# Performance work log

Measured on AMD Instinct MI355X. Metric: run time of the kernel, lower is better.

## Reference

```python
import jax, jax.numpy as jnp
import numpy as np

N_NODES = 50000
N_EDGES = 800000
IN_CH = 256
HID = 64
HEADS = 4
OUT_CH = 4
NEG_SLOPE = 0.2


def _add_self_loops(edge_index, n):
    ar = jnp.arange(n, dtype=edge_index.dtype)
    loops = jnp.stack([ar, ar])
    return jnp.concatenate([edge_index, loops], axis=1)


def _gat_conv(x, edge_index, W, att_src, att_dst, bias, heads, ch):
    # PyG GATConv (no edge features, add_self_loops=True, concat=True)
    n = x.shape[0]
    ei = _add_self_loops(edge_index, n)
    src, dst = ei[0], ei[1]
    xp = (x @ W).reshape(n, heads, ch)            # [N,H,C]
    a_src = (xp * att_src).sum(-1)                 # [N,H]
    a_dst = (xp * att_dst).sum(-1)                 # [N,H]
    alpha = jax.nn.leaky_relu(a_src[src] + a_dst[dst], NEG_SLOPE)  # [E',H]
    amax = jax.ops.segment_max(alpha, dst, num_segments=n)
    alpha = jnp.exp(alpha - amax[dst])
    denom = jax.ops.segment_sum(alpha, dst, num_segments=n)
    alpha = alpha / (denom[dst] + 1e-16)
    msg = xp[src] * alpha[:, :, None]              # [E',H,C]
    out = jax.ops.segment_sum(msg, dst, num_segments=n)  # [N,H,C]
    return out.reshape(n, heads * ch) + bias


def setup_inputs() -> dict:
    key = jax.random.key(0)
    ks = jax.random.split(key, 12)
    x = jax.random.normal(ks[0], (N_NODES, IN_CH), dtype=jnp.float32)
    edge_index = jax.random.randint(ks[1], (2, N_EDGES), 0, N_NODES, dtype=jnp.int64)
    w = jax.random.uniform(ks[2], (N_EDGES,), dtype=jnp.float32)
    s1 = 1.0 / np.sqrt(IN_CH)
    s2 = 1.0 / np.sqrt(HEADS * HID)
    return {
        "x": x, "edge_index": edge_index, "w": w,
        "W1": jax.random.normal(ks[3], (IN_CH, HEADS * HID), dtype=jnp.float32) * s1,
        "att_src1": jax.random.normal(ks[4], (1, HEADS, HID), dtype=jnp.float32) * s2,
        "att_dst1": jax.random.normal(ks[5], (1, HEADS, HID), dtype=jnp.float32) * s2,
        "b1": jnp.zeros((HEADS * HID,), dtype=jnp.float32),
        "W2": jax.random.normal(ks[6], (HEADS * HID, HID), dtype=jnp.float32) * s2,
        "att_src2": jax.random.normal(ks[7], (1, 1, HID), dtype=jnp.float32) * s2,
        "att_dst2": jax.random.normal(ks[8], (1, 1, HID), dtype=jnp.float32) * s2,
        "b2": jnp.zeros((HID,), dtype=jnp.float32),
        "Wc": jax.random.normal(ks[9], (2 * HID, OUT_CH), dtype=jnp.float32) * (1.0 / np.sqrt(2 * HID)),
        "bc": jnp.zeros((OUT_CH,), dtype=jnp.float32),
    }


def reference(x, edge_index, w, W1, att_src1, att_dst1, b1,
              W2, att_src2, att_dst2, b2, Wc, bc):
    # w (edge_attr) is ignored: GATConv was built without edge_dim, so no lin_edge.
    h = _gat_conv(x, edge_index, W1, att_src1, att_dst1, b1, HEADS, HID)
    h = jax.nn.relu(h)
    h = _gat_conv(h, edge_index, W2, att_src2, att_dst2, b2, 1, HID)
    row, col = edge_index[0], edge_index[1]
    edge_emb = jnp.concatenate([h[row], h[col]], axis=-1)  # [E, 2*HID]
    return edge_emb @ Wc + bc
```

## Files before the change

### kernel.cpp

```cpp
#include <hip/hip_runtime.h>


#define NEG 0.2f

typedef __attribute__((ext_vector_type(8))) short bf16x8;
typedef __attribute__((ext_vector_type(4))) float f32x4;

__device__ __forceinline__ unsigned short f2bf(float f) {
    unsigned int u = __float_as_uint(f);
    unsigned int r = (u + 0x7FFFu + ((u >> 16) & 1u)) >> 16;
    return (unsigned short)r;
}
__device__ __forceinline__ float bf2f(unsigned short h) {
    return __uint_as_float(((unsigned int)h) << 16);
}
__device__ __forceinline__ float bflo(unsigned int u) { return __uint_as_float(u << 16); }
__device__ __forceinline__ float bfhi(unsigned int u) { return __uint_as_float(u & 0xFFFF0000u); }
__device__ __forceinline__ float lrelu(float x) { return x > 0.f ? x : NEG * x; }

__device__ __forceinline__ void async16(const void* g, void* l) {
    __builtin_amdgcn_global_load_lds(
        (const __attribute__((address_space(1))) unsigned int*)g,
        (__attribute__((address_space(3))) unsigned int*)l, 16, 0, 0);
}


__global__ __launch_bounds__(256) void k_init(int* deg, int* cur, int n) {
    int i = blockIdx.x * 256 + threadIdx.x;
    if (i < n) { deg[i] = 1; cur[i] = 0; }
}

__global__ __launch_bounds__(256) void k_hist(const int* __restrict__ ei, int* deg, int E) {
    int e = blockIdx.x * 256 + threadIdx.x;
    if (e < E) atomicAdd(&deg[ei[E + e]], 1);
}

__global__ __launch_bounds__(256) void k_bsum(const int* __restrict__ deg, int* __restrict__ bsum, int n) {
    int i = blockIdx.x * 256 + threadIdx.x;
    int v = (i < n) ? deg[i] : 0;
#pragma unroll
    for (int off = 1; off < 64; off <<= 1) v += __shfl_xor(v, off, 64);
    __shared__ int ws[4];
    int wv = threadIdx.x >> 6, l = threadIdx.x & 63;
    if (l == 0) ws[wv] = v;
    __syncthreads();
    if (threadIdx.x == 0) bsum[blockIdx.x] = ws[0] + ws[1] + ws[2] + ws[3];
}

__global__ __launch_bounds__(256) void k_bscan(const int* __restrict__ bsum, int* __restrict__ boff,
                                               int* __restrict__ rowptr, int nb, int n) {
    __shared__ int s[256];
    int t = threadIdx.x;
    int v = (t < nb) ? bsum[t] : 0;
    s[t] = v;
    __syncthreads();
    for (int off = 1; off < 256; off <<= 1) {
        int u = (t >= off) ? s[t - off] : 0;
        __syncthreads();
        s[t] += u;
        __syncthreads();
    }
    if (t < nb) boff[t] = s[t] - v;
    if (t == nb - 1) rowptr[n] = s[t];
}

__global__ __launch_bounds__(256) void k_rowptr(const int* __restrict__ deg, const int* __restrict__ boff,
                                                int* __restrict__ rowptr, int n) {
    __shared__ int s[256];
    int i = blockIdx.x * 256 + threadIdx.x;
    int t = threadIdx.x;
    int v = (i < n) ? deg[i] : 0;
    s[t] = v;
    __syncthreads();
    for (int off = 1; off < 256; off <<= 1) {
        int u = (t >= off) ? s[t - off] : 0;
        __syncthreads();
        s[t] += u;
        __syncthreads();
    }
    if (i < n) rowptr[i] = boff[blockIdx.x] + s[t] - v;
}

__global__ __launch_bounds__(256) void k_scatter(const int* __restrict__ ei, const int* __restrict__ rowptr,
                                                 int* cur, int* csr_src, int E, int N) {
    int e = blockIdx.x * 256 + threadIdx.x;
    if (e < E) {
        int d = ei[E + e];
        int pos = rowptr[d] + atomicAdd(&cur[d], 1);
        csr_src[pos] = ei[e];
    } else if (e < E + N) {
        int i = e - E;
        int pos = rowptr[i] + atomicAdd(&cur[i], 1);
        csr_src[pos] = i;
    }
}


__global__ __launch_bounds__(256) void k_pack_hi(const float* __restrict__ src,
                                                 unsigned short* __restrict__ hi, long n4) {
    long i = (long)blockIdx.x * 256 + threadIdx.x;
    long stride = (long)gridDim.x * 256;
    for (; i < n4; i += stride) {
        float4 v = ((const float4*)src)[i];
        ((ushort4*)hi)[i] = make_ushort4(f2bf(v.x), f2bf(v.y), f2bf(v.z), f2bf(v.w));
    }
}

__global__ __launch_bounds__(256) void k_pack_w2(const float* __restrict__ W1,
                                                 const float* __restrict__ W2,
                                                 unsigned short* __restrict__ W1hT,
                                                 unsigned short* __restrict__ W1lT,
                                                 unsigned short* __restrict__ W2hT,
                                                 unsigned short* __restrict__ W2lT) {
    int t = blockIdx.x * 256 + threadIdx.x;
    if (t < 256 * 256) {
        int n = t >> 8, k = t & 255;
        float v = W1[k * 256 + n];
        unsigned short h = f2bf(v);
        W1hT[t] = h;
        W1lT[t] = f2bf(v - bf2f(h));
    } else {
        int t2 = t - 256 * 256;
        if (t2 < 64 * 256) {
            int n = t2 >> 8, k = t2 & 255;
            float v = W2[k * 64 + n];
            unsigned short h = f2bf(v);
            W2hT[t2] = h;
            W2lT[t2] = f2bf(v - bf2f(h));
        }
    }
}

template<int WGM, int WGN>
__global__ __launch_bounds__(256, 2) void k_gemm_lds(const unsigned short* __restrict__ Ah,
                                                     const unsigned short* __restrict__ BhT,
                                                     const unsigned short* __restrict__ BlT,
                                                     unsigned short* __restrict__ Cb, int M, int N, int K,
                                                     const float* __restrict__ att_s,
                                                     const float* __restrict__ att_d,
                                                     float* __restrict__ as, float* __restrict__ ad, int H) {
    constexpr int BM = WGM * 64, BN = WGN * 64;
    __shared__ char lds[BM * 128 + BN * 256];
    char* LAh = lds;
    char* LBh = lds + BM * 128;
    char* LBl = lds + BM * 128 + BN * 128;

    const int t = threadIdx.x, wv = t >> 6, l = t & 63;
    const int r = l & 15, hk = l >> 4;
    const int m0 = blockIdx.x * BM;
    const int n0 = blockIdx.y * BN;
    const int wr = wv / WGN, wc = wv % WGN;
    const int wrow0 = wr * 64, wcol0 = wc * 64;

    f32x4 acc[4][4];
#pragma unroll
    for (int i = 0; i < 4; i++)
#pragma unroll
        for (int j = 0; j < 4; j++) acc[i][j] = f32x4{0, 0, 0, 0};

    const int lrow8 = l >> 3;
    const int cbs = ((l & 7) ^ lrow8) << 4;
    const size_t K2 = (size_t)K * 2;
    const int NCH = K >> 6;

    for (int c = 0; c < NCH; ++c) {
        const int kk2 = c * 128;
        {
            const int SA = BM / 8;
            for (int i = wv; i < SA; i += 4) {
                int row = i * 8 + lrow8;
                size_t go = (size_t)(m0 + row) * K2 + kk2 + cbs;
                async16((const char*)Ah + go, LAh + i * 1024);
            }
            const int SB = BN / 8;
            for (int i = wv; i < SB; i += 4) {
                int row = i * 8 + lrow8;
                size_t go = (size_t)(n0 + row) * K2 + kk2 + cbs;
                async16((const char*)BhT + go, LBh + i * 1024);
                async16((const char*)BlT + go, LBl + i * 1024);
            }
        }
        __syncthreads();
#pragma unroll
        for (int ks = 0; ks < 2; ++ks) {
            const int cb = ks * 64 + hk * 16;
            bf16x8 a_h[4], b_h[4], b_l[4];
#pragma unroll
            for (int fm = 0; fm < 4; ++fm) {
                int row = wrow0 + fm * 16 + r;
                int ad_ = row * 128 + (cb ^ ((row & 7) << 4));
                a_h[fm] = *(const bf16x8*)(LAh + ad_);
            }
#pragma unroll
            for (int fn = 0; fn < 4; ++fn) {
                int row = wcol0 + fn * 16 + r;
                int ad_ = row * 128 + (cb ^ ((row & 7) << 4));
                b_h[fn] = *(const bf16x8*)(LBh + ad_);
                b_l[fn] = *(const bf16x8*)(LBl + ad_);
            }
#pragma unroll
            for (int fm = 0; fm < 4; ++fm)
#pragma unroll
                for (int fn = 0; fn < 4; ++fn) {
                    acc[fm][fn] = __builtin_amdgcn_mfma_f32_16x16x32_bf16(a_h[fm], b_h[fn], acc[fm][fn], 0, 0, 0);
                    acc[fm][fn] = __builtin_amdgcn_mfma_f32_16x16x32_bf16(a_h[fm], b_l[fn], acc[fm][fn], 0, 0, 0);
                }
        }
        if (c + 1 < NCH) __syncthreads();
    }

#pragma unroll
    for (int fm = 0; fm < 4; ++fm)
#pragma unroll
        for (int fn = 0; fn < 4; ++fn)
#pragma unroll
            for (int j = 0; j < 4; ++j) {
                int m = m0 + wrow0 + fm * 16 + hk * 4 + j;
                if (m < M) Cb[(size_t)m * N + n0 + wcol0 + fn * 16 + r] = f2bf(acc[fm][fn][j]);
            }

    {
        int head = (n0 + wcol0) >> 6;
        float satt[4], datt[4];
#pragma unroll
        for (int fn = 0; fn < 4; ++fn) {
            satt[fn] = att_s[head * 64 + fn * 16 + r];
            datt[fn] = att_d[head * 64 + fn * 16 + r];
        }
#pragma unroll
        for (int fm = 0; fm < 4; ++fm)
#pragma unroll
            for (int j = 0; j < 4; ++j) {
                float ps = 0.f, pd = 0.f;
#pragma unroll
                for (int fn = 0; fn < 4; ++fn) {
                    ps += satt[fn] * acc[fm][fn][j];
                    pd += datt[fn] * acc[fm][fn][j];
                }
#pragma unroll
                for (int off = 1; off <= 8; off <<= 1) {
                    ps += __shfl_xor(ps, off, 64);
                    pd += __shfl_xor(pd, off, 64);
                }
                if (r == 0) {
                    int m = m0 + wrow0 + fm * 16 + hk * 4 + j;
                    if (m < M) { as[m * H + head] = ps; ad[m * H + head] = pd; }
                }
            }
    }
}


__global__ __launch_bounds__(256) void k_gather1(const unsigned short* __restrict__ xpb,
                                                 const float* __restrict__ as, const float* __restrict__ ad,
                                                 const int* __restrict__ rowptr, const int* __restrict__ csr_src,
                                                 const float* __restrict__ b1,
                                                 unsigned short* __restrict__ h1h, int M) {
    int wv = threadIdx.x >> 6, lane = threadIdx.x & 63;
    int n = blockIdx.x * 4 + wv;
    if (n >= M) return;
    int half = lane >> 5;
    int q = lane & 31;
    int h = q >> 3;
    float adv = ad[n * 4 + h];
    int start = rowptr[n], end = rowptr[n + 1];
    float acc[8] = {0.f, 0.f, 0.f, 0.f, 0.f, 0.f, 0.f, 0.f};
    float den = 0.f;

    auto edge = [&](int s, uint4 v) {
        float p = __expf(lrelu(as[s * 4 + h] + adv));
        den += p;
        acc[0] += p * bflo(v.x); acc[1] += p * bfhi(v.x);
        acc[2] += p * bflo(v.y); acc[3] += p * bfhi(v.y);
        acc[4] += p * bflo(v.z); acc[5] += p * bfhi(v.z);
        acc[6] += p * bflo(v.w); acc[7] += p * bfhi(v.w);
    };

    int e = start;
    for (; e + 7 < end; e += 8) {
        int sa = csr_src[e + half];
        int sb = csr_src[e + 2 + half];
        int sc = csr_src[e + 4 + half];
        int sd = csr_src[e + 6 + half];
        uint4 va = *(const uint4*)(xpb + (size_t)sa * 256 + q * 8);
        uint4 vb = *(const uint4*)(xpb + (size_t)sb * 256 + q * 8);
        uint4 vc = *(const uint4*)(xpb + (size_t)sc * 256 + q * 8);
        uint4 vd = *(const uint4*)(xpb + (size_t)sd * 256 + q * 8);
        edge(sa, va); edge(sb, vb); edge(sc, vc); edge(sd, vd);
    }
    if (e + 3 < end) {
        int sa = csr_src[e + half];
        int sb = csr_src[e + 2 + half];
        uint4 va = *(const uint4*)(xpb + (size_t)sa * 256 + q * 8);
        uint4 vb = *(const uint4*)(xpb + (size_t)sb * 256 + q * 8);
        edge(sa, va); edge(sb, vb);
        e += 4;
    }
    if (e + 1 < end) {
        int sa = csr_src[e + half];
        uint4 va = *(const uint4*)(xpb + (size_t)sa * 256 + q * 8);
        edge(sa, va);
        e += 2;
    }
    if (e < end && half == 0) {
        int sa = csr_src[e];
        uint4 va = *(const uint4*)(xpb + (size_t)sa * 256 + q * 8);
        edge(sa, va);
    }

#pragma unroll
    for (int j = 0; j < 8; j++) acc[j] += __shfl_xor(acc[j], 32, 64);
    den += __shfl_xor(den, 32, 64);

    float dinv = 1.f / (den + 1e-16f);
    float4 b0 = *(const float4*)(b1 + q * 8);
    float4 b4 = *(const float4*)(b1 + q * 8 + 4);
    float o0 = fmaxf(acc[0] * dinv + b0.x, 0.f);
    float o1 = fmaxf(acc[1] * dinv + b0.y, 0.f);
    float o2 = fmaxf(acc[2] * dinv + b0.z, 0.f);
    float o3 = fmaxf(acc[3] * dinv + b0.w, 0.f);
    float o4 = fmaxf(acc[4] * dinv + b4.x, 0.f);
    float o5 = fmaxf(acc[5] * dinv + b4.y, 0.f);
    float o6 = fmaxf(acc[6] * dinv + b4.z, 0.f);
    float o7 = fmaxf(acc[7] * dinv + b4.w, 0.f);
    if (half == 0) {
        uint4 Hv;
        Hv.x = (unsigned)f2bf(o0) | ((unsigned)f2bf(o1) << 16);
        Hv.y = (unsigned)f2bf(o2) | ((unsigned)f2bf(o3) << 16);
        Hv.z = (unsigned)f2bf(o4) | ((unsigned)f2bf(o5) << 16);
        Hv.w = (unsigned)f2bf(o6) | ((unsigned)f2bf(o7) << 16);
        *(uint4*)(h1h + (size_t)n * 256 + q * 8) = Hv;
    }
}

__global__ __launch_bounds__(256) void k_gather2(const unsigned short* __restrict__ xp2b,
                                                 const float* __restrict__ as, const float* __restrict__ ad,
                                                 const int* __restrict__ rowptr, const int* __restrict__ csr_src,
                                                 const float* __restrict__ b2, const float* __restrict__ Wc,
                                                 float* __restrict__ uv, int M) {
    int wv = threadIdx.x >> 6, lane = threadIdx.x & 63;
    int n = blockIdx.x * 4 + wv;
    if (n >= M) return;
    int g = lane >> 4, q = lane & 15;
    float adv = ad[n];
    int start = rowptr[n], end = rowptr[n + 1];
    float acc[4] = {0.f, 0.f, 0.f, 0.f};
    float den = 0.f;
    for (int e = start; e < end; e += 4) {
        int ee = e + g;
        bool ok = ee < end;
        int s = csr_src[ok ? ee : start];
        uint2 v = *(const uint2*)(xp2b + (size_t)s * 64 + q * 4);
        float pw = ok ? __expf(lrelu(as[s] + adv)) : 0.f;
        den += pw;
        acc[0] += pw * bflo(v.x); acc[1] += pw * bfhi(v.x);
        acc[2] += pw * bflo(v.y); acc[3] += pw * bfhi(v.y);
    }
#pragma unroll
    for (int j = 0; j < 4; j++) {
        acc[j] += __shfl_xor(acc[j], 16, 64);
        acc[j] += __shfl_xor(acc[j], 32, 64);
    }
    den += __shfl_xor(den, 16, 64);
    den += __shfl_xor(den, 32, 64);
    float dinv = 1.f / (den + 1e-16f);
    float pr[8] = {0.f, 0.f, 0.f, 0.f, 0.f, 0.f, 0.f, 0.f};
#pragma unroll
    for (int j = 0; j < 4; j++) {
        int c = q * 4 + j;
        float val = acc[j] * dinv + b2[c];
#pragma unroll
        for (int k = 0; k < 4; k++) {
            pr[k]     += val * Wc[c * 4 + k];
            pr[4 + k] += val * Wc[(64 + c) * 4 + k];
        }
    }
#pragma unroll
    for (int off = 1; off <= 8; off <<= 1)
#pragma unroll
        for (int j = 0; j < 8; j++) pr[j] += __shfl_xor(pr[j], off, 64);
    if (lane == 0) {
        float4* o = (float4*)(uv + (size_t)n * 8);
        o[0] = make_float4(pr[0], pr[1], pr[2], pr[3]);
        o[1] = make_float4(pr[4], pr[5], pr[6], pr[7]);
    }
}

__global__ __launch_bounds__(256) void k_classify(const int* __restrict__ ei, const float* __restrict__ uv,
                                                  const float* __restrict__ bc, float* __restrict__ out, int E) {
    int e = blockIdx.x * 256 + threadIdx.x;
    if (e >= E) return;
    int r = ei[e];
    int c = ei[E + e];
    float4 u = *(const float4*)(uv + (size_t)r * 8);
    float4 v = *(const float4*)(uv + (size_t)c * 8 + 4);
    float4 o;
    o.x = u.x + v.x + bc[0];
    o.y = u.y + v.y + bc[1];
    o.z = u.z + v.z + bc[2];
    o.w = u.w + v.w + bc[3];
    *(float4*)(out + (size_t)e * 4) = o;
}


extern "C" void kernel_launch(void* const* d_in, const int* in_sizes, int n_in,
                              void* d_out, int out_size, void* d_ws, size_t ws_size,
                              hipStream_t stream) {
    const float* x    = (const float*)d_in[0];
    const int*   ei   = (const int*)d_in[1];
    const float* W1   = (const float*)d_in[3];
    const float* atS1 = (const float*)d_in[4];
    const float* atD1 = (const float*)d_in[5];
    const float* b1   = (const float*)d_in[6];
    const float* W2   = (const float*)d_in[7];
    const float* atS2 = (const float*)d_in[8];
    const float* atD2 = (const float*)d_in[9];
    const float* b2   = (const float*)d_in[10];
    const float* Wc   = (const float*)d_in[11];
    const float* bc   = (const float*)d_in[12];
    float* out = (float*)d_out;

    const int Nn = in_sizes[0] / 256;
    const int E = in_sizes[1] / 2;
    const int Etot = E + Nn;
    const int NB = (Nn + 255) / 256;

    char* w = (char*)d_ws;
    size_t off = 0;
    auto alloc = [&](size_t b) { size_t o = off; off = (o + b + 255) & ~(size_t)255; return o; };
    size_t oXH  = alloc((size_t)Nn * 256 * 2);
    size_t oXPB = alloc((size_t)Nn * 256 * 2);
    size_t oAS1 = alloc((size_t)Nn * 4 * 4);
    size_t oAD1 = alloc((size_t)Nn * 4 * 4);
    size_t oDEG = alloc((size_t)Nn * 4);
    size_t oCUR = alloc((size_t)Nn * 4);
    size_t oRP  = alloc((size_t)(Nn + 1) * 4);
    size_t oCSR = alloc((size_t)Etot * 4);
    size_t oW1H = alloc((size_t)256 * 256 * 2);
    size_t oW1L = alloc((size_t)256 * 256 * 2);
    size_t oW2H = alloc((size_t)256 * 64 * 2);
    size_t oW2L = alloc((size_t)256 * 64 * 2);
    size_t oBS  = alloc((size_t)NB * 4);
    size_t oBO  = alloc((size_t)NB * 4);
    (void)ws_size;

    unsigned short* xh   = (unsigned short*)(w + oXH);
    unsigned short* h1h  = (unsigned short*)(w + oXH);
    unsigned short* xpb  = (unsigned short*)(w + oXPB);
    unsigned short* xp2b = (unsigned short*)(w + oXPB);
    float* uv  = (float*)(w + oXPB + (size_t)Nn * 64 * 2 + 256);
    uv = (float*)(((uintptr_t)uv + 255) & ~(uintptr_t)255);
    float* as1 = (float*)(w + oAS1);
    float* ad1 = (float*)(w + oAD1);
    float* as2 = (float*)(w + oAS1);
    float* ad2 = (float*)(w + oAD1);
    int* deg    = (int*)(w + oDEG);
    int* cur    = (int*)(w + oCUR);
    int* rowptr = (int*)(w + oRP);
    int* csr    = (int*)(w + oCSR);
    int* bsum   = (int*)(w + oBS);
    int* boff   = (int*)(w + oBO);
    unsigned short* W1hT = (unsigned short*)(w + oW1H);
    unsigned short* W1lT = (unsigned short*)(w + oW1L);
    unsigned short* W2hT = (unsigned short*)(w + oW2H);
    unsigned short* W2lT = (unsigned short*)(w + oW2L);

    k_init<<<NB, 256, 0, stream>>>(deg, cur, Nn);
    k_hist<<<(E + 255) / 256, 256, 0, stream>>>(ei, deg, E);
    k_bsum<<<NB, 256, 0, stream>>>(deg, bsum, Nn);
    k_bscan<<<1, 256, 0, stream>>>(bsum, boff, rowptr, NB, Nn);
    k_rowptr<<<NB, 256, 0, stream>>>(deg, boff, rowptr, Nn);
    k_scatter<<<(Etot + 255) / 256, 256, 0, stream>>>(ei, rowptr, cur, csr, E, Nn);

    k_pack_hi<<<2048, 256, 0, stream>>>(x, xh, (long)Nn * 64);
    k_pack_w2<<<(256 * 256 + 64 * 256 + 255) / 256, 256, 0, stream>>>(W1, W2, W1hT, W1lT, W2hT, W2lT);

    {
        dim3 g((Nn + 127) / 128, 2);
        k_gemm_lds<2, 2><<<g, 256, 0, stream>>>(xh, W1hT, W1lT, xpb, Nn, 256, 256,
                                                atS1, atD1, as1, ad1, 4);
    }
    k_gather1<<<(Nn + 3) / 4, 256, 0, stream>>>(xpb, as1, ad1, rowptr, csr, b1, h1h, Nn);

    {
        dim3 g((Nn + 255) / 256, 1);
        k_gemm_lds<4, 1><<<g, 256, 0, stream>>>(h1h, W2hT, W2lT, xp2b, Nn, 64, 256,
                                                atS2, atD2, as2, ad2, 1);
    }
    k_gather2<<<(Nn + 3) / 4, 256, 0, stream>>>(xp2b, as2, ad2, rowptr, csr, b2, Wc, uv, Nn);

    k_classify<<<(E + 255) / 256, 256, 0, stream>>>(ei, uv, bc, out, E);
}
```

Measured before the change: 282.0 us.

## Fuse degree histogram and bf16 packing into one prep kernel; unroll gather2

Merges the degree histogram, the x-to-bf16 pack and the W1/W2 transpose-split pack into a single block-partitioned k_prep launch. The two init stores are replaced by memsets, and the self-loop +1 is folded into the scan kernels. This cuts kernel launches and lets the independent prep work run concurrently. The layer-2 gather loop is also unrolled by two with separate accumulators to keep more loads in flight. The prep grid is fixed at 2368 blocks, so the W pack branch relies on exact sizing and has no bounds check.

```diff
diff --git a/kernel.cpp b/kernel.cpp
--- a/kernel.cpp
+++ b/kernel.cpp
@@ -24,20 +24,44 @@
         (__attribute__((address_space(3))) unsigned int*)l, 16, 0, 0);
 }
 
-
-__global__ __launch_bounds__(256) void k_init(int* deg, int* cur, int n) {
-    int i = blockIdx.x * 256 + threadIdx.x;
-    if (i < n) { deg[i] = 1; cur[i] = 0; }
-}
-
-__global__ __launch_bounds__(256) void k_hist(const int* __restrict__ ei, int* deg, int E) {
-    int e = blockIdx.x * 256 + threadIdx.x;
-    if (e < E) atomicAdd(&deg[ei[E + e]], 1);
-}
+__global__ __launch_bounds__(256) void k_prep(const int* __restrict__ ei, int* __restrict__ deg, int E,
+                                              const float* __restrict__ x, unsigned short* __restrict__ xh,
+                                              long n4,
+                                              const float* __restrict__ W1, const float* __restrict__ W2,
+                                              unsigned short* __restrict__ W1hT, unsigned short* __restrict__ W1lT,
+                                              unsigned short* __restrict__ W2hT, unsigned short* __restrict__ W2lT) {
+    int b = blockIdx.x;
+    if (b < 1024) {
+        for (long e = (long)b * 256 + threadIdx.x; e < E; e += (long)1024 * 256)
+            atomicAdd(&deg[ei[E + e]], 1);
+    } else if (b < 2048) {
+        for (long i = (long)(b - 1024) * 256 + threadIdx.x; i < n4; i += (long)1024 * 256) {
+            float4 v = ((const float4*)x)[i];
+            ((ushort4*)xh)[i] = make_ushort4(f2bf(v.x), f2bf(v.y), f2bf(v.z), f2bf(v.w));
+        }
+    } else {
+        int t = (b - 2048) * 256 + threadIdx.x;
+        if (t < 256 * 256) {
+            int n = t >> 8, k = t & 255;
+            float v = W1[k * 256 + n];
+            unsigned short h = f2bf(v);
+            W1hT[t] = h;
+            W1lT[t] = f2bf(v - bf2f(h));
+        } else {
+            int t2 = t - 256 * 256;
+            int n = t2 >> 8, k = t2 & 255;
+            float v = W2[k * 64 + n];
+            unsigned short h = f2bf(v);
+            W2hT[t2] = h;
+            W2lT[t2] = f2bf(v - bf2f(h));
+        }
+    }
+}
+
 
 __global__ __launch_bounds__(256) void k_bsum(const int* __restrict__ deg, int* __restrict__ bsum, int n) {
     int i = blockIdx.x * 256 + threadIdx.x;
-    int v = (i < n) ? deg[i] : 0;
+    int v = (i < n) ? deg[i] + 1 : 0;
 #pragma unroll
     for (int off = 1; off < 64; off <<= 1) v += __shfl_xor(v, off, 64);
     __shared__ int ws[4];
@@ -69,7 +93,7 @@
     __shared__ int s[256];
     int i = blockIdx.x * 256 + threadIdx.x;
     int t = threadIdx.x;
-    int v = (i < n) ? deg[i] : 0;
+    int v = (i < n) ? deg[i] + 1 : 0;
     s[t] = v;
     __syncthreads();
     for (int off = 1; off < 256; off <<= 1) {
@@ -92,42 +116,6 @@
         int i = e - E;
         int pos = rowptr[i] + atomicAdd(&cur[i], 1);
         csr_src[pos] = i;
-    }
-}
-
-
-__global__ __launch_bounds__(256) void k_pack_hi(const float* __restrict__ src,
-                                                 unsigned short* __restrict__ hi, long n4) {
-    long i = (long)blockIdx.x * 256 + threadIdx.x;
-    long stride = (long)gridDim.x * 256;
-    for (; i < n4; i += stride) {
-        float4 v = ((const float4*)src)[i];
-        ((ushort4*)hi)[i] = make_ushort4(f2bf(v.x), f2bf(v.y), f2bf(v.z), f2bf(v.w));
-    }
-}
-
-__global__ __launch_bounds__(256) void k_pack_w2(const float* __restrict__ W1,
-                                                 const float* __restrict__ W2,
-                                                 unsigned short* __restrict__ W1hT,
-                                                 unsigned short* __restrict__ W1lT,
-                                                 unsigned short* __restrict__ W2hT,
-                                                 unsigned short* __restrict__ W2lT) {
-    int t = blockIdx.x * 256 + threadIdx.x;
-    if (t < 256 * 256) {
-        int n = t >> 8, k = t & 255;
-        float v = W1[k * 256 + n];
-        unsigned short h = f2bf(v);
-        W1hT[t] = h;
-        W1lT[t] = f2bf(v - bf2f(h));
-    } else {
-        int t2 = t - 256 * 256;
-        if (t2 < 64 * 256) {
-            int n = t2 >> 8, k = t2 & 255;
-            float v = W2[k * 64 + n];
-            unsigned short h = f2bf(v);
-            W2hT[t2] = h;
-            W2lT[t2] = f2bf(v - bf2f(h));
-        }
     }
 }
 
@@ -344,23 +332,40 @@
     int g = lane >> 4, q = lane & 15;
     float adv = ad[n];
     int start = rowptr[n], end = rowptr[n + 1];
-    float acc[4] = {0.f, 0.f, 0.f, 0.f};
-    float den = 0.f;
-    for (int e = start; e < end; e += 4) {
+    float acc0[4] = {0.f, 0.f, 0.f, 0.f}, acc1[4] = {0.f, 0.f, 0.f, 0.f};
+    float den0 = 0.f, den1 = 0.f;
+    int e = start;
+    for (; e + 7 < end; e += 8) {
+        int s0 = csr_src[e + g];
+        int s1 = csr_src[e + 4 + g];
+        uint2 v0 = *(const uint2*)(xp2b + (size_t)s0 * 64 + q * 4);
+        uint2 v1 = *(const uint2*)(xp2b + (size_t)s1 * 64 + q * 4);
+        float p0 = __expf(lrelu(as[s0] + adv));
+        float p1 = __expf(lrelu(as[s1] + adv));
+        den0 += p0; den1 += p1;
+        acc0[0] += p0 * bflo(v0.x); acc0[1] += p0 * bfhi(v0.x);
+        acc0[2] += p0 * bflo(v0.y); acc0[3] += p0 * bfhi(v0.y);
+        acc1[0] += p1 * bflo(v1.x); acc1[1] += p1 * bfhi(v1.x);
+        acc1[2] += p1 * bflo(v1.y); acc1[3] += p1 * bfhi(v1.y);
+    }
+    for (; e < end; e += 4) {
         int ee = e + g;
         bool ok = ee < end;
         int s = csr_src[ok ? ee : start];
         uint2 v = *(const uint2*)(xp2b + (size_t)s * 64 + q * 4);
         float pw = ok ? __expf(lrelu(as[s] + adv)) : 0.f;
-        den += pw;
-        acc[0] += pw * bflo(v.x); acc[1] += pw * bfhi(v.x);
-        acc[2] += pw * bflo(v.y); acc[3] += pw * bfhi(v.y);
-    }
+        den0 += pw;
+        acc0[0] += pw * bflo(v.x); acc0[1] += pw * bfhi(v.x);
+        acc0[2] += pw * bflo(v.y); acc0[3] += pw * bfhi(v.y);
+    }
+    float acc[4];
 #pragma unroll
     for (int j = 0; j < 4; j++) {
+        acc[j] = acc0[j] + acc1[j];
         acc[j] += __shfl_xor(acc[j], 16, 64);
         acc[j] += __shfl_xor(acc[j], 32, 64);
     }
+    float den = den0 + den1;
     den += __shfl_xor(den, 16, 64);
     den += __shfl_xor(den, 32, 64);
     float dinv = 1.f / (den + 1e-16f);
@@ -465,16 +470,17 @@
     unsigned short* W2hT = (unsigned short*)(w + oW2H);
     unsigned short* W2lT = (unsigned short*)(w + oW2L);
 
-    k_init<<<NB, 256, 0, stream>>>(deg, cur, Nn);
-    k_hist<<<(E + 255) / 256, 256, 0, stream>>>(ei, deg, E);
+    hipMemsetAsync(deg, 0, (size_t)Nn * 4, stream);
+    hipMemsetAsync(cur, 0, (size_t)Nn * 4, stream);
+
+    k_prep<<<2368, 256, 0, stream>>>(ei, deg, E, x, xh, (long)Nn * 64,
+                                     W1, W2, W1hT, W1lT, W2hT, W2lT);
+
     k_bsum<<<NB, 256, 0, stream>>>(deg, bsum, Nn);
     k_bscan<<<1, 256, 0, stream>>>(bsum, boff, rowptr, NB, Nn);
     k_rowptr<<<NB, 256, 0, stream>>>(deg, boff, rowptr, Nn);
     k_scatter<<<(Etot + 255) / 256, 256, 0, stream>>>(ei, rowptr, cur, csr, E, Nn);
 
-    k_pack_hi<<<2048, 256, 0, stream>>>(x, xh, (long)Nn * 64);
-    k_pack_w2<<<(256 * 256 + 64 * 256 + 255) / 256, 256, 0, stream>>>(W1, W2, W1hT, W1lT, W2hT, W2lT);
-
     {
         dim3 g((Nn + 127) / 128, 2);
         k_gemm_lds<2, 2><<<g, 256, 0, stream>>>(xh, W1hT, W1lT, xpb, Nn, 256, 256,
```

Result: faster. 271.6 us (-3.7%).
